# Kernel tuning notes

Hardware: AMD Instinct MI355X
Metric: run time of the kernel (lower is better)

Reference implementation:

```python
import jax, jax.numpy as jnp
import numpy as np

HEADS = 8
EPS = 1e-5


def _layernorm(x, g, b):
    mu = jnp.mean(x, axis=-1, keepdims=True)
    var = jnp.mean(jnp.square(x - mu), axis=-1, keepdims=True)
    return (x - mu) * jax.lax.rsqrt(var + EPS) * g + b


def setup_inputs() -> dict:
    key = jax.random.key(0)
    ks = jax.random.split(key, 10)
    B, S, D = 4, 2048, 256
    d_ff = 2 * D
    s = 0.02
    return {
        "x": jax.random.normal(ks[0], (B, S, D), dtype=jnp.float32),
        "ln1_g": jnp.ones((D,), jnp.float32),
        "ln1_b": jnp.zeros((D,), jnp.float32),
        "w_qkv": jax.random.normal(ks[1], (3 * D, D), jnp.float32) * s,
        "b_qkv": jnp.zeros((3 * D,), jnp.float32),
        "w_proj": jax.random.normal(ks[2], (D, D), jnp.float32) * s,
        "b_proj": jnp.zeros((D,), jnp.float32),
        "ln2_g": jnp.ones((D,), jnp.float32),
        "ln2_b": jnp.zeros((D,), jnp.float32),
        "w1": jax.random.normal(ks[3], (d_ff, D), jnp.float32) * s,
        "b1": jnp.zeros((d_ff,), jnp.float32),
        "w2": jax.random.normal(ks[4], (D, d_ff), jnp.float32) * s,
        "b2": jnp.zeros((D,), jnp.float32),
    }


def reference(x, ln1_g, ln1_b, w_qkv, b_qkv, w_proj, b_proj,
              ln2_g, ln2_b, w1, b1, w2, b2):
    B, S, D = x.shape
    H = HEADS
    dh = D // H
    scale = dh ** -0.5

    # --- attention sublayer (pre-LN) ---
    y = _layernorm(x, ln1_g, ln1_b)
    qkv = y @ w_qkv.T + b_qkv                       # [B,S,3D]
    qkv = qkv.reshape(B, S, 3, H, dh)
    q = jnp.transpose(qkv[:, :, 0], (0, 2, 1, 3))   # [B,H,S,dh]
    k = jnp.transpose(qkv[:, :, 1], (0, 2, 1, 3))
    v = jnp.transpose(qkv[:, :, 2], (0, 2, 1, 3))
    attn = jax.nn.softmax(jnp.einsum('bhsd,bhtd->bhst', q, k) * scale, axis=-1)
    ctx = jnp.einsum('bhst,bhtd->bhsd', attn, v)    # [B,H,S,dh]
    ctx = jnp.transpose(ctx, (0, 2, 1, 3)).reshape(B, S, D)
    x = x + ctx @ w_proj.T + b_proj

    # --- FFN sublayer (pre-LN) ---
    y = _layernorm(x, ln2_g, ln2_b)
    h = jax.nn.silu(y @ w1.T + b1)                  # [B,S,2D]
    x = x + h @ w2.T + b2
    return x
```

## Files before the change

### kernel.cpp

```cpp
#include <hip/hip_runtime.h>
#include <cstddef>

constexpr int kB   = 4;
constexpr int kS   = 2048;
constexpr int kD   = 256;
constexpr int kH   = 8;
constexpr int kDH  = 32;
constexpr int kDFF = 512;
constexpr int kM   = kB * kS;
constexpr float kEps = 1e-5f;
constexpr float kScaleL2E = 0.17677669529663687f * 1.4426950408889634f;

typedef float f32x4  __attribute__((ext_vector_type(4)));
typedef short bf16x8 __attribute__((ext_vector_type(8)));
typedef unsigned short u16;
typedef unsigned int   u32;

__device__ inline u16 f2bf(float x) {
    union { float f; unsigned u; } c; c.f = x;
    const unsigned r = c.u + 0x7fffu + ((c.u >> 16) & 1u);
    return (u16)(r >> 16);
}

__device__ inline u32 pk_trunc(float lo, float hi) {
    union { float f; u32 u; } a, b; a.f = lo; b.f = hi;
    return __builtin_amdgcn_perm(b.u, a.u, 0x07060302u);
}

__device__ inline size_t pkoff(int row, int col, int nkb) {
    return ((size_t)(row >> 4) * nkb + (col >> 5)) * 512
         + (row & 15) * 32 + (col & 31);
}

__global__ __launch_bounds__(256)
void conv_w_kernel(const float* __restrict__ wq, const float* __restrict__ wp,
                   const float* __restrict__ w1, const float* __restrict__ w2,
                   u16* __restrict__ dst)
{
    const int e0 = (blockIdx.x * 256 + threadIdx.x) * 4;
    const float* src; int off, K, base;
    if (e0 < 196608)      { src = wq; off = e0;          K = 256; base = 0; }
    else if (e0 < 262144) { src = wp; off = e0 - 196608; K = 256; base = 196608; }
    else if (e0 < 393216) { src = w1; off = e0 - 262144; K = 256; base = 262144; }
    else                  { src = w2; off = e0 - 393216; K = 512; base = 393216; }
    const float4 v = *(const float4*)&src[off];
    const int n = off / K, k = off - n * K;
    const size_t po = pkoff(n, k, K >> 5);
    *(ushort4*)&dst[base + po] = make_ushort4(f2bf(v.x), f2bf(v.y), f2bf(v.z), f2bf(v.w));
}

__global__ __launch_bounds__(256)
void ln_kernel(const float* __restrict__ x, const float* __restrict__ g,
               const float* __restrict__ b, u16* __restrict__ y)
{
    const int wave = threadIdx.x >> 6;
    const int lane = threadIdx.x & 63;
    const int row  = blockIdx.x * 4 + wave;
    const float4 v = *(const float4*)&x[(size_t)row * kD + lane * 4];
    float s1 = (v.x + v.y) + (v.z + v.w);
    float s2 = (v.x * v.x + v.y * v.y) + (v.z * v.z + v.w * v.w);
    #pragma unroll
    for (int off = 1; off < 64; off <<= 1) {
        s1 += __shfl_xor(s1, off);
        s2 += __shfl_xor(s2, off);
    }
    const float mu  = s1 * (1.0f / kD);
    const float var = s2 * (1.0f / kD) - mu * mu;
    const float inv = rsqrtf(var + kEps);
    const float4 g4 = *(const float4*)&g[lane * 4];
    const float4 b4 = *(const float4*)&b[lane * 4];
    *(ushort4*)&y[pkoff(row, lane * 4, kD >> 5)] = make_ushort4(
        f2bf((v.x - mu) * inv * g4.x + b4.x),
        f2bf((v.y - mu) * inv * g4.y + b4.y),
        f2bf((v.z - mu) * inv * g4.z + b4.z),
        f2bf((v.w - mu) * inv * g4.w + b4.w));
}

template<int NI, int OUTMODE, bool RES, int KTOT>
__global__ __launch_bounds__(256)
void gemm_pk(const u16* __restrict__ Ap, const u16* __restrict__ Wp,
             const float* __restrict__ bias, const float* __restrict__ res,
             float* __restrict__ Cf, u16* __restrict__ Cb,
             u16* __restrict__ KbP, u16* __restrict__ VtP, int N)
{
    constexpr int NK = KTOT / 32;
    const int tid  = threadIdx.x;
    const int wave = tid >> 6;
    const int lane = tid & 63;
    const int quad = lane >> 4;
    const int l16  = lane & 15;
    const int m0 = blockIdx.x * 128;
    const int n0 = blockIdx.y * (NI * 16);
    const int fo = l16 * 32 + quad * 8;

    f32x4 acc[2][NI];
    #pragma unroll
    for (int mt = 0; mt < 2; ++mt)
        #pragma unroll
        for (int ni = 0; ni < NI; ++ni) acc[mt][ni] = {0.f, 0.f, 0.f, 0.f};

    const u16* a0p = Ap + (size_t)((m0 >> 4) + wave)     * NK * 512 + fo;
    const u16* a1p = Ap + (size_t)((m0 >> 4) + 4 + wave) * NK * 512 + fo;
    const u16* wp  = Wp + (size_t)(n0 >> 4)              * NK * 512 + fo;

    #pragma unroll 2
    for (int k = 0; k < NK; ++k) {
        const bf16x8 a0 = *(const bf16x8*)&a0p[k * 512];
        const bf16x8 a1 = *(const bf16x8*)&a1p[k * 512];
        #pragma unroll
        for (int ni = 0; ni < NI; ++ni) {
            const bf16x8 wf = *(const bf16x8*)&wp[((size_t)ni * NK + k) * 512];
            acc[0][ni] = __builtin_amdgcn_mfma_f32_16x16x32_bf16(a0, wf, acc[0][ni], 0, 0, 0);
            acc[1][ni] = __builtin_amdgcn_mfma_f32_16x16x32_bf16(a1, wf, acc[1][ni], 0, 0, 0);
        }
    }

    #pragma unroll
    for (int mt = 0; mt < 2; ++mt) {
        #pragma unroll
        for (int ni = 0; ni < NI; ++ni) {
            const float bias_v = bias[n0 + ni * 16 + l16];
            #pragma unroll
            for (int r = 0; r < 4; ++r) {
                const int m = m0 + mt * 64 + wave * 16 + quad * 4 + r;
                const int n = n0 + ni * 16 + l16;
                float v = acc[mt][ni][r] + bias_v;
                if (OUTMODE == 0) {
                    if (RES) v += res[(size_t)m * N + n];
                    Cf[(size_t)m * N + n] = v;
                } else if (OUTMODE == 1) {
                    v = v / (1.0f + __expf(-v));
                    Cb[pkoff(m, n, kDFF >> 5)] = f2bf(v);
                } else {
                    const int rgn = n0 >> 8;
                    const int nl  = n & 255;
                    const int hh  = nl >> 5, dh = nl & 31;
                    const int bb  = m >> 11, s = m & (kS - 1);
                    const int bh  = bb * kH + hh;
                    if (rgn == 0)
                        Cb[((size_t)bh * kS + s) * kDH + dh] = f2bf(v * kScaleL2E);
                    else if (rgn == 1)
                        KbP[((size_t)bh * kS + s) * kDH + dh] = f2bf(v);
                    else {
                        const int so = s & 31;
                        const int vq = (so >> 2) & 3;
                        const int vj = (so & 3) | (((so >> 4) & 1) << 2);
                        VtP[(((size_t)bh * (kS / 32) + (s >> 5)) * 4 + vq) * 256
                            + dh * 8 + vj] = f2bf(v);
                    }
                }
            }
        }
    }
}

__global__ __launch_bounds__(256)
void attn_kernel(const u16* __restrict__ Qb, const u16* __restrict__ Kb,
                 const u16* __restrict__ Vp, u16* __restrict__ ctx)
{
    __shared__ float cbuf[2][64 * 33];
    const int tid  = threadIdx.x;
    const int wave = tid >> 6;
    const int lane = tid & 63;
    const int quad = lane >> 4;
    const int l16  = lane & 15;
    const int h = blockIdx.y;
    const int b = blockIdx.z;
    const int bh = b * kH + h;
    const int qsub = wave >> 1;
    const int half = wave & 1;
    const int q0 = blockIdx.x * 128 + qsub * 64;

    bf16x8 aq[4];
    #pragma unroll
    for (int qb = 0; qb < 4; ++qb)
        aq[qb] = *(const bf16x8*)
            &Qb[((size_t)bh * kS + q0 + qb * 16 + l16) * kDH + quad * 8];

    const u16* Kbase = Kb + (size_t)bh * kS * kDH;
    const u16* Vbase = Vp + (size_t)bh * (kS * 32);

    f32x4 O[4][2] = {};
    f32x4 lsum[4] = {};
    const f32x4 zz = {0.f, 0.f, 0.f, 0.f};
    union { u32 u[4]; bf16x8 v; } ones;
    ones.u[0] = ones.u[1] = ones.u[2] = ones.u[3] = 0x3F803F80u;

    auto load_tile = [&](int kt, bf16x8 (&kf)[4], bf16x8 (&vf)[2][2]) {
        #pragma unroll
        for (int kg = 0; kg < 4; ++kg)
            kf[kg] = *(const bf16x8*)
                &Kbase[(size_t)(kt + kg * 16 + l16) * kDH + quad * 8];
        #pragma unroll
        for (int ks = 0; ks < 2; ++ks)
            #pragma unroll
            for (int nf = 0; nf < 2; ++nf)
                vf[ks][nf] = *(const bf16x8*)
                    &Vbase[(size_t)(((kt >> 5) + ks) * 4 + quad) * 1024
                           + (nf * 16 + l16) * 8];
    };

    auto comp_tile = [&](bf16x8 (&kf)[4], bf16x8 (&vf)[2][2]) {
        #pragma unroll
        for (int qb = 0; qb < 4; ++qb) {
            f32x4 S0 = __builtin_amdgcn_mfma_f32_16x16x32_bf16(kf[0], aq[qb], zz, 0, 0, 0);
            f32x4 S1 = __builtin_amdgcn_mfma_f32_16x16x32_bf16(kf[1], aq[qb], zz, 0, 0, 0);
            f32x4 S2 = __builtin_amdgcn_mfma_f32_16x16x32_bf16(kf[2], aq[qb], zz, 0, 0, 0);
            f32x4 S3 = __builtin_amdgcn_mfma_f32_16x16x32_bf16(kf[3], aq[qb], zz, 0, 0, 0);

            union { u32 u[4]; bf16x8 v; } pA0, pA1;
            pA0.u[0] = pk_trunc(__builtin_amdgcn_exp2f(S0[0]), __builtin_amdgcn_exp2f(S0[1]));
            pA0.u[1] = pk_trunc(__builtin_amdgcn_exp2f(S0[2]), __builtin_amdgcn_exp2f(S0[3]));
            pA0.u[2] = pk_trunc(__builtin_amdgcn_exp2f(S1[0]), __builtin_amdgcn_exp2f(S1[1]));
            pA0.u[3] = pk_trunc(__builtin_amdgcn_exp2f(S1[2]), __builtin_amdgcn_exp2f(S1[3]));
            pA1.u[0] = pk_trunc(__builtin_amdgcn_exp2f(S2[0]), __builtin_amdgcn_exp2f(S2[1]));
            pA1.u[1] = pk_trunc(__builtin_amdgcn_exp2f(S2[2]), __builtin_amdgcn_exp2f(S2[3]));
            pA1.u[2] = pk_trunc(__builtin_amdgcn_exp2f(S3[0]), __builtin_amdgcn_exp2f(S3[1]));
            pA1.u[3] = pk_trunc(__builtin_amdgcn_exp2f(S3[2]), __builtin_amdgcn_exp2f(S3[3]));

            lsum[qb] = __builtin_amdgcn_mfma_f32_16x16x32_bf16(pA0.v, ones.v, lsum[qb], 0, 0, 0);
            lsum[qb] = __builtin_amdgcn_mfma_f32_16x16x32_bf16(pA1.v, ones.v, lsum[qb], 0, 0, 0);

            O[qb][0] = __builtin_amdgcn_mfma_f32_16x16x32_bf16(pA0.v, vf[0][0], O[qb][0], 0, 0, 0);
            O[qb][1] = __builtin_amdgcn_mfma_f32_16x16x32_bf16(pA0.v, vf[0][1], O[qb][1], 0, 0, 0);
            O[qb][0] = __builtin_amdgcn_mfma_f32_16x16x32_bf16(pA1.v, vf[1][0], O[qb][0], 0, 0, 0);
            O[qb][1] = __builtin_amdgcn_mfma_f32_16x16x32_bf16(pA1.v, vf[1][1], O[qb][1], 0, 0, 0);
        }
    };

    const int kbeg = half * (kS / 2);
    #pragma unroll 1
    for (int t2 = 0; t2 < 8; ++t2) {
        const int ktA = kbeg + t2 * 128;
        bf16x8 kfA[4], vfA[2][2], kfB[4], vfB[2][2];
        load_tile(ktA,      kfA, vfA);
        load_tile(ktA + 64, kfB, vfB);
        comp_tile(kfA, vfA);
        comp_tile(kfB, vfB);
    }

    float* cb = cbuf[qsub];
    if (half == 1) {
        #pragma unroll
        for (int qb = 0; qb < 4; ++qb)
            #pragma unroll
            for (int r = 0; r < 4; ++r) {
                const int row = qb * 16 + quad * 4 + r;
                cb[row * 33 + l16]      = O[qb][0][r];
                cb[row * 33 + 16 + l16] = O[qb][1][r];
                if (l16 == 0)
                    cb[row * 33 + 32] = lsum[qb][r];
            }
    }
    __syncthreads();
    if (half == 0) {
        #pragma unroll
        for (int qb = 0; qb < 4; ++qb)
            #pragma unroll
            for (int r = 0; r < 4; ++r) {
                const int row = qb * 16 + quad * 4 + r;
                const float lq  = lsum[qb][r] + cb[row * 33 + 32];
                const float inv = 1.0f / lq;
                const float o0 = O[qb][0][r] + cb[row * 33 + l16];
                const float o1 = O[qb][1][r] + cb[row * 33 + 16 + l16];
                const int q = q0 + row;
                const int mrow = b * kS + q;
                u16* crow = ctx + ((size_t)(mrow >> 4) * (kD >> 5) + h) * 512
                          + (mrow & 15) * 32;
                crow[l16]      = f2bf(o0 * inv);
                crow[16 + l16] = f2bf(o1 * inv);
            }
    }
}

extern "C" void kernel_launch(void* const* d_in, const int* in_sizes, int n_in,
                              void* d_out, int out_size, void* d_ws, size_t ws_size,
                              hipStream_t stream)
{
    const float* x      = (const float*)d_in[0];
    const float* ln1_g  = (const float*)d_in[1];
    const float* ln1_b  = (const float*)d_in[2];
    const float* w_qkv  = (const float*)d_in[3];
    const float* b_qkv  = (const float*)d_in[4];
    const float* w_proj = (const float*)d_in[5];
    const float* b_proj = (const float*)d_in[6];
    const float* ln2_g  = (const float*)d_in[7];
    const float* ln2_b  = (const float*)d_in[8];
    const float* w1     = (const float*)d_in[9];
    const float* b1     = (const float*)d_in[10];
    const float* w2     = (const float*)d_in[11];
    const float* b2     = (const float*)d_in[12];
    float* out = (float*)d_out;

    char* ws = (char*)d_ws;
    u16* Qb  = (u16*)ws;
    u16* Kb  = (u16*)(ws + ((size_t)4  << 20));
    u16* Vp  = (u16*)(ws + ((size_t)8  << 20));
    u16* ctx = (u16*)(ws + ((size_t)12 << 20));
    u16* y   = (u16*)(ws + ((size_t)16 << 20));
    u16* h   = (u16*)ws;
    u16* Wb  = (u16*)(ws + ((size_t)20 << 20));
    u16* wqb = Wb;
    u16* wpb = Wb + 196608;
    u16* w1b = Wb + 262144;
    u16* w2b = Wb + 393216;

    const dim3 blk(256);

    conv_w_kernel<<<dim3(512), blk, 0, stream>>>(w_qkv, w_proj, w1, w2, Wb);
    ln_kernel<<<dim3(kM / 4), blk, 0, stream>>>(x, ln1_g, ln1_b, y);
    gemm_pk<4, 2, false, 256><<<dim3(kM / 128, 12), blk, 0, stream>>>(
        y, wqb, b_qkv, nullptr, nullptr, Qb, Kb, Vp, 0);
    attn_kernel<<<dim3(kS / 128, kH, kB), blk, 0, stream>>>(Qb, Kb, Vp, ctx);
    gemm_pk<2, 0, true, 256><<<dim3(kM / 128, kD / 32), blk, 0, stream>>>(
        ctx, wpb, b_proj, x, out, nullptr, nullptr, nullptr, kD);
    ln_kernel<<<dim3(kM / 4), blk, 0, stream>>>(out, ln2_g, ln2_b, y);
    gemm_pk<4, 1, false, 256><<<dim3(kM / 128, kDFF / 64), blk, 0, stream>>>(
        y, w1b, b1, nullptr, nullptr, h, nullptr, nullptr, kDFF);
    gemm_pk<2, 0, true, 512><<<dim3(kM / 128, kD / 32), blk, 0, stream>>>(
        h, w2b, b2, out, out, nullptr, nullptr, nullptr, kD);
}
```

Before: 162.1 us.

## Keep weight fragments in registers across M tiles and fuse weight conversion into LN

The GEMM kernel now preloads each block's full weight fragments (NI x NK bf16x8) into registers once, then loops over two M tiles, reusing them instead of re-reading weights from global memory for every k step. The N tile width is reduced (NI 4->2 or 2->1) to keep register use manageable, and the grid changes accordingly. The weight conversion is folded into the first LayerNorm launch as extra blocks, saving one kernel launch. The register-held weights raise VGPR pressure and may cut occupancy, and A-tile loads are still streamed from global memory.

```diff
diff --git a/kernel.cpp b/kernel.cpp
--- a/kernel.cpp
+++ b/kernel.cpp
@@ -8,6 +8,7 @@
 constexpr int kDH  = 32;
 constexpr int kDFF = 512;
 constexpr int kM   = kB * kS;
+constexpr int kMT  = kM / 128;
 constexpr float kEps = 1e-5f;
 constexpr float kScaleL2E = 0.17677669529663687f * 1.4426950408889634f;
 
@@ -33,26 +34,26 @@
 }
 
 __global__ __launch_bounds__(256)
-void conv_w_kernel(const float* __restrict__ wq, const float* __restrict__ wp,
-                   const float* __restrict__ w1, const float* __restrict__ w2,
-                   u16* __restrict__ dst)
+void prep_kernel(const float* __restrict__ x, const float* __restrict__ g,
+                 const float* __restrict__ b, u16* __restrict__ y,
+                 const float* __restrict__ wq, const float* __restrict__ wp,
+                 const float* __restrict__ w1, const float* __restrict__ w2,
+                 u16* __restrict__ wdst)
 {
-    const int e0 = (blockIdx.x * 256 + threadIdx.x) * 4;
-    const float* src; int off, K, base;
-    if (e0 < 196608)      { src = wq; off = e0;          K = 256; base = 0; }
-    else if (e0 < 262144) { src = wp; off = e0 - 196608; K = 256; base = 196608; }
-    else if (e0 < 393216) { src = w1; off = e0 - 262144; K = 256; base = 262144; }
-    else                  { src = w2; off = e0 - 393216; K = 512; base = 393216; }
-    const float4 v = *(const float4*)&src[off];
-    const int n = off / K, k = off - n * K;
-    const size_t po = pkoff(n, k, K >> 5);
-    *(ushort4*)&dst[base + po] = make_ushort4(f2bf(v.x), f2bf(v.y), f2bf(v.z), f2bf(v.w));
-}
-
-__global__ __launch_bounds__(256)
-void ln_kernel(const float* __restrict__ x, const float* __restrict__ g,
-               const float* __restrict__ b, u16* __restrict__ y)
-{
+    if (blockIdx.x >= kM / 4) {
+        const int e0 = ((blockIdx.x - kM / 4) * 256 + threadIdx.x) * 4;
+        const float* src; int off, K, base;
+        if (e0 < 196608)      { src = wq; off = e0;          K = 256; base = 0; }
+        else if (e0 < 262144) { src = wp; off = e0 - 196608; K = 256; base = 196608; }
+        else if (e0 < 393216) { src = w1; off = e0 - 262144; K = 256; base = 262144; }
+        else                  { src = w2; off = e0 - 393216; K = 512; base = 393216; }
+        const float4 v = *(const float4*)&src[off];
+        const int n = off / K, k = off - n * K;
+        const size_t po = pkoff(n, k, K >> 5);
+        *(ushort4*)&wdst[base + po] =
+            make_ushort4(f2bf(v.x), f2bf(v.y), f2bf(v.z), f2bf(v.w));
+        return;
+    }
     const int wave = threadIdx.x >> 6;
     const int lane = threadIdx.x & 63;
     const int row  = blockIdx.x * 4 + wave;
@@ -76,77 +77,91 @@
         f2bf((v.w - mu) * inv * g4.w + b4.w));
 }
 
-template<int NI, int OUTMODE, bool RES, int KTOT>
+template<int NI, int OUTMODE, bool RES, int KTOT, int MT>
 __global__ __launch_bounds__(256)
-void gemm_pk(const u16* __restrict__ Ap, const u16* __restrict__ Wp,
+void gemm_ps(const u16* __restrict__ Ap, const u16* __restrict__ Wp,
              const float* __restrict__ bias, const float* __restrict__ res,
              float* __restrict__ Cf, u16* __restrict__ Cb,
              u16* __restrict__ KbP, u16* __restrict__ VtP, int N)
 {
     constexpr int NK = KTOT / 32;
+    constexpr int GX = kMT / MT;
     const int tid  = threadIdx.x;
     const int wave = tid >> 6;
     const int lane = tid & 63;
     const int quad = lane >> 4;
     const int l16  = lane & 15;
-    const int m0 = blockIdx.x * 128;
     const int n0 = blockIdx.y * (NI * 16);
     const int fo = l16 * 32 + quad * 8;
 
-    f32x4 acc[2][NI];
+    bf16x8 wfr[NI][NK];
     #pragma unroll
-    for (int mt = 0; mt < 2; ++mt)
-        #pragma unroll
-        for (int ni = 0; ni < NI; ++ni) acc[mt][ni] = {0.f, 0.f, 0.f, 0.f};
-
-    const u16* a0p = Ap + (size_t)((m0 >> 4) + wave)     * NK * 512 + fo;
-    const u16* a1p = Ap + (size_t)((m0 >> 4) + 4 + wave) * NK * 512 + fo;
-    const u16* wp  = Wp + (size_t)(n0 >> 4)              * NK * 512 + fo;
-
-    #pragma unroll 2
-    for (int k = 0; k < NK; ++k) {
-        const bf16x8 a0 = *(const bf16x8*)&a0p[k * 512];
-        const bf16x8 a1 = *(const bf16x8*)&a1p[k * 512];
-        #pragma unroll
-        for (int ni = 0; ni < NI; ++ni) {
-            const bf16x8 wf = *(const bf16x8*)&wp[((size_t)ni * NK + k) * 512];
-            acc[0][ni] = __builtin_amdgcn_mfma_f32_16x16x32_bf16(a0, wf, acc[0][ni], 0, 0, 0);
-            acc[1][ni] = __builtin_amdgcn_mfma_f32_16x16x32_bf16(a1, wf, acc[1][ni], 0, 0, 0);
+    for (int ni = 0; ni < NI; ++ni)
+        #pragma unroll
+        for (int k = 0; k < NK; ++k)
+            wfr[ni][k] = *(const bf16x8*)
+                &Wp[(size_t)((n0 >> 4) + ni) * NK * 512 + (size_t)k * 512 + fo];
+
+    float biasv[NI];
+    #pragma unroll
+    for (int ni = 0; ni < NI; ++ni) biasv[ni] = bias[n0 + ni * 16 + l16];
+
+    #pragma unroll 1
+    for (int t = 0; t < MT; ++t) {
+        const int m0 = (blockIdx.x + t * GX) * 128;
+
+        f32x4 acc[2][NI];
+        #pragma unroll
+        for (int mt = 0; mt < 2; ++mt)
+            #pragma unroll
+            for (int ni = 0; ni < NI; ++ni) acc[mt][ni] = {0.f, 0.f, 0.f, 0.f};
+
+        const u16* a0p = Ap + (size_t)((m0 >> 4) + wave)     * NK * 512 + fo;
+        const u16* a1p = Ap + (size_t)((m0 >> 4) + 4 + wave) * NK * 512 + fo;
+
+        #pragma unroll 4
+        for (int k = 0; k < NK; ++k) {
+            const bf16x8 a0 = *(const bf16x8*)&a0p[(size_t)k * 512];
+            const bf16x8 a1 = *(const bf16x8*)&a1p[(size_t)k * 512];
+            #pragma unroll
+            for (int ni = 0; ni < NI; ++ni) {
+                acc[0][ni] = __builtin_amdgcn_mfma_f32_16x16x32_bf16(a0, wfr[ni][k], acc[0][ni], 0, 0, 0);
+                acc[1][ni] = __builtin_amdgcn_mfma_f32_16x16x32_bf16(a1, wfr[ni][k], acc[1][ni], 0, 0, 0);
+            }
         }
-    }
-
-    #pragma unroll
-    for (int mt = 0; mt < 2; ++mt) {
-        #pragma unroll
-        for (int ni = 0; ni < NI; ++ni) {
-            const float bias_v = bias[n0 + ni * 16 + l16];
-            #pragma unroll
-            for (int r = 0; r < 4; ++r) {
-                const int m = m0 + mt * 64 + wave * 16 + quad * 4 + r;
-                const int n = n0 + ni * 16 + l16;
-                float v = acc[mt][ni][r] + bias_v;
-                if (OUTMODE == 0) {
-                    if (RES) v += res[(size_t)m * N + n];
-                    Cf[(size_t)m * N + n] = v;
-                } else if (OUTMODE == 1) {
-                    v = v / (1.0f + __expf(-v));
-                    Cb[pkoff(m, n, kDFF >> 5)] = f2bf(v);
-                } else {
-                    const int rgn = n0 >> 8;
-                    const int nl  = n & 255;
-                    const int hh  = nl >> 5, dh = nl & 31;
-                    const int bb  = m >> 11, s = m & (kS - 1);
-                    const int bh  = bb * kH + hh;
-                    if (rgn == 0)
-                        Cb[((size_t)bh * kS + s) * kDH + dh] = f2bf(v * kScaleL2E);
-                    else if (rgn == 1)
-                        KbP[((size_t)bh * kS + s) * kDH + dh] = f2bf(v);
-                    else {
-                        const int so = s & 31;
-                        const int vq = (so >> 2) & 3;
-                        const int vj = (so & 3) | (((so >> 4) & 1) << 2);
-                        VtP[(((size_t)bh * (kS / 32) + (s >> 5)) * 4 + vq) * 256
-                            + dh * 8 + vj] = f2bf(v);
+
+        #pragma unroll
+        for (int mt = 0; mt < 2; ++mt) {
+            #pragma unroll
+            for (int ni = 0; ni < NI; ++ni) {
+                #pragma unroll
+                for (int r = 0; r < 4; ++r) {
+                    const int m = m0 + mt * 64 + wave * 16 + quad * 4 + r;
+                    const int n = n0 + ni * 16 + l16;
+                    float v = acc[mt][ni][r] + biasv[ni];
+                    if (OUTMODE == 0) {
+                        if (RES) v += res[(size_t)m * N + n];
+                        Cf[(size_t)m * N + n] = v;
+                    } else if (OUTMODE == 1) {
+                        v = v / (1.0f + __expf(-v));
+                        Cb[pkoff(m, n, kDFF >> 5)] = f2bf(v);
+                    } else {
+                        const int rgn = n0 >> 8;
+                        const int nl  = n & 255;
+                        const int hh  = nl >> 5, dh = nl & 31;
+                        const int bb  = m >> 11, s = m & (kS - 1);
+                        const int bh  = bb * kH + hh;
+                        if (rgn == 0)
+                            Cb[((size_t)bh * kS + s) * kDH + dh] = f2bf(v * kScaleL2E);
+                        else if (rgn == 1)
+                            KbP[((size_t)bh * kS + s) * kDH + dh] = f2bf(v);
+                        else {
+                            const int so = s & 31;
+                            const int vq = (so >> 2) & 3;
+                            const int vj = (so & 3) | (((so >> 4) & 1) << 2);
+                            VtP[(((size_t)bh * (kS / 32) + (s >> 5)) * 4 + vq) * 256
+                                + dh * 8 + vj] = f2bf(v);
+                        }
                     }
                 }
             }
@@ -307,16 +322,17 @@
 
     const dim3 blk(256);
 
-    conv_w_kernel<<<dim3(512), blk, 0, stream>>>(w_qkv, w_proj, w1, w2, Wb);
-    ln_kernel<<<dim3(kM / 4), blk, 0, stream>>>(x, ln1_g, ln1_b, y);
-    gemm_pk<4, 2, false, 256><<<dim3(kM / 128, 12), blk, 0, stream>>>(
+    prep_kernel<<<dim3(kM / 4 + 512), blk, 0, stream>>>(
+        x, ln1_g, ln1_b, y, w_qkv, w_proj, w1, w2, Wb);
+    gemm_ps<2, 2, false, 256, 2><<<dim3(kMT / 2, 24), blk, 0, stream>>>(
         y, wqb, b_qkv, nullptr, nullptr, Qb, Kb, Vp, 0);
     attn_kernel<<<dim3(kS / 128, kH, kB), blk, 0, stream>>>(Qb, Kb, Vp, ctx);
-    gemm_pk<2, 0, true, 256><<<dim3(kM / 128, kD / 32), blk, 0, stream>>>(
+    gemm_ps<2, 0, true, 256, 2><<<dim3(kMT / 2, 8), blk, 0, stream>>>(
         ctx, wpb, b_proj, x, out, nullptr, nullptr, nullptr, kD);
-    ln_kernel<<<dim3(kM / 4), blk, 0, stream>>>(out, ln2_g, ln2_b, y);
-    gemm_pk<4, 1, false, 256><<<dim3(kM / 128, kDFF / 64), blk, 0, stream>>>(
+    prep_kernel<<<dim3(kM / 4), blk, 0, stream>>>(
+        out, ln2_g, ln2_b, y, nullptr, nullptr, nullptr, nullptr, nullptr);
+    gemm_ps<2, 1, false, 256, 2><<<dim3(kMT / 2, 16), blk, 0, stream>>>(
         y, w1b, b1, nullptr, nullptr, h, nullptr, nullptr, kDFF);
-    gemm_pk<2, 0, true, 512><<<dim3(kM / 128, kD / 32), blk, 0, stream>>>(
+    gemm_ps<1, 0, true, 512, 2><<<dim3(kMT / 2, 16), blk, 0, stream>>>(
         h, w2b, b2, out, out, nullptr, nullptr, nullptr, kD);
 }
```

Result: slower. 207.1 us (+27.8%).

## Fuse weight conversion with LN1, and output projection with residual and LN2

Applied to the files above, without the earlier changes.

Merges the weight bf16 conversion and the first layernorm into one launch by giving extra blocks the conversion work. Replaces the projection GEMM plus separate LN2 kernel with a single kernel in which each wave computes 16 full rows of 256 columns via MFMA, adds bias and residual, writes out, then does row reduction and LN2 in registers. This removes two launches and the round trip of the projection output through memory before LN2. In exchange, the new projection kernel reads weights straight from global memory without LDS tiling and uses a 128-block grid, which may cut occupancy and weight reuse.

```diff
diff --git a/kernel.cpp b/kernel.cpp
--- a/kernel.cpp
+++ b/kernel.cpp
@@ -33,26 +33,26 @@
 }
 
 __global__ __launch_bounds__(256)
-void conv_w_kernel(const float* __restrict__ wq, const float* __restrict__ wp,
-                   const float* __restrict__ w1, const float* __restrict__ w2,
-                   u16* __restrict__ dst)
-{
-    const int e0 = (blockIdx.x * 256 + threadIdx.x) * 4;
-    const float* src; int off, K, base;
-    if (e0 < 196608)      { src = wq; off = e0;          K = 256; base = 0; }
-    else if (e0 < 262144) { src = wp; off = e0 - 196608; K = 256; base = 196608; }
-    else if (e0 < 393216) { src = w1; off = e0 - 262144; K = 256; base = 262144; }
-    else                  { src = w2; off = e0 - 393216; K = 512; base = 393216; }
-    const float4 v = *(const float4*)&src[off];
-    const int n = off / K, k = off - n * K;
-    const size_t po = pkoff(n, k, K >> 5);
-    *(ushort4*)&dst[base + po] = make_ushort4(f2bf(v.x), f2bf(v.y), f2bf(v.z), f2bf(v.w));
-}
-
-__global__ __launch_bounds__(256)
-void ln_kernel(const float* __restrict__ x, const float* __restrict__ g,
-               const float* __restrict__ b, u16* __restrict__ y)
-{
+void prep_kernel(const float* __restrict__ x, const float* __restrict__ g,
+                 const float* __restrict__ b, u16* __restrict__ y,
+                 const float* __restrict__ wq, const float* __restrict__ wp,
+                 const float* __restrict__ w1, const float* __restrict__ w2,
+                 u16* __restrict__ wdst)
+{
+    if (blockIdx.x >= kM / 4) {
+        const int e0 = ((blockIdx.x - kM / 4) * 256 + threadIdx.x) * 4;
+        const float* src; int off, K, base;
+        if (e0 < 196608)      { src = wq; off = e0;          K = 256; base = 0; }
+        else if (e0 < 262144) { src = wp; off = e0 - 196608; K = 256; base = 196608; }
+        else if (e0 < 393216) { src = w1; off = e0 - 262144; K = 256; base = 262144; }
+        else                  { src = w2; off = e0 - 393216; K = 512; base = 393216; }
+        const float4 v = *(const float4*)&src[off];
+        const int n = off / K, k = off - n * K;
+        const size_t po = pkoff(n, k, K >> 5);
+        *(ushort4*)&wdst[base + po] =
+            make_ushort4(f2bf(v.x), f2bf(v.y), f2bf(v.z), f2bf(v.w));
+        return;
+    }
     const int wave = threadIdx.x >> 6;
     const int lane = threadIdx.x & 63;
     const int row  = blockIdx.x * 4 + wave;
@@ -155,6 +155,70 @@
 }
 
 __global__ __launch_bounds__(256)
+void proj_ln2_kernel(const u16* __restrict__ ctx, const u16* __restrict__ Wp,
+                     const float* __restrict__ bias, const float* __restrict__ x,
+                     const float* __restrict__ g, const float* __restrict__ bb,
+                     float* __restrict__ out, u16* __restrict__ y)
+{
+    const int tid  = threadIdx.x;
+    const int wave = tid >> 6;
+    const int lane = tid & 63;
+    const int quad = lane >> 4;
+    const int l16  = lane & 15;
+    const int tr   = blockIdx.x * 4 + wave;
+    const int fo   = l16 * 32 + quad * 8;
+
+    f32x4 acc[16];
+    #pragma unroll
+    for (int ni = 0; ni < 16; ++ni) acc[ni] = {0.f, 0.f, 0.f, 0.f};
+
+    const u16* ap = ctx + (size_t)tr * 8 * 512 + fo;
+    #pragma unroll 2
+    for (int k = 0; k < 8; ++k) {
+        const bf16x8 a = *(const bf16x8*)&ap[k * 512];
+        #pragma unroll
+        for (int ni = 0; ni < 16; ++ni) {
+            const bf16x8 wf = *(const bf16x8*)&Wp[((size_t)ni * 8 + k) * 512 + fo];
+            acc[ni] = __builtin_amdgcn_mfma_f32_16x16x32_bf16(a, wf, acc[ni], 0, 0, 0);
+        }
+    }
+
+    float bv[16], gv[16], bbv[16];
+    #pragma unroll
+    for (int ni = 0; ni < 16; ++ni) {
+        bv[ni]  = bias[ni * 16 + l16];
+        gv[ni]  = g[ni * 16 + l16];
+        bbv[ni] = bb[ni * 16 + l16];
+    }
+
+    const int m0 = tr * 16;
+    #pragma unroll
+    for (int r = 0; r < 4; ++r) {
+        const int m = m0 + quad * 4 + r;
+        float v[16], s1 = 0.f, s2 = 0.f;
+        #pragma unroll
+        for (int ni = 0; ni < 16; ++ni) {
+            v[ni] = acc[ni][r] + bv[ni] + x[(size_t)m * kD + ni * 16 + l16];
+            out[(size_t)m * kD + ni * 16 + l16] = v[ni];
+            s1 += v[ni];
+            s2 += v[ni] * v[ni];
+        }
+        s1 += __shfl_xor(s1, 1); s2 += __shfl_xor(s2, 1);
+        s1 += __shfl_xor(s1, 2); s2 += __shfl_xor(s2, 2);
+        s1 += __shfl_xor(s1, 4); s2 += __shfl_xor(s2, 4);
+        s1 += __shfl_xor(s1, 8); s2 += __shfl_xor(s2, 8);
+        const float mu  = s1 * (1.0f / kD);
+        const float var = s2 * (1.0f / kD) - mu * mu;
+        const float inv = rsqrtf(var + kEps);
+        u16* yb = y + (size_t)tr * 8 * 512 + (quad * 4 + r) * 32 + l16;
+        #pragma unroll
+        for (int ni = 0; ni < 16; ++ni)
+            yb[(ni >> 1) * 512 + (ni & 1) * 16] =
+                f2bf((v[ni] - mu) * inv * gv[ni] + bbv[ni]);
+    }
+}
+
+__global__ __launch_bounds__(256)
 void attn_kernel(const u16* __restrict__ Qb, const u16* __restrict__ Kb,
                  const u16* __restrict__ Vp, u16* __restrict__ ctx)
 {
@@ -307,14 +371,13 @@
 
     const dim3 blk(256);
 
-    conv_w_kernel<<<dim3(512), blk, 0, stream>>>(w_qkv, w_proj, w1, w2, Wb);
-    ln_kernel<<<dim3(kM / 4), blk, 0, stream>>>(x, ln1_g, ln1_b, y);
+    prep_kernel<<<dim3(kM / 4 + 512), blk, 0, stream>>>(
+        x, ln1_g, ln1_b, y, w_qkv, w_proj, w1, w2, Wb);
     gemm_pk<4, 2, false, 256><<<dim3(kM / 128, 12), blk, 0, stream>>>(
         y, wqb, b_qkv, nullptr, nullptr, Qb, Kb, Vp, 0);
     attn_kernel<<<dim3(kS / 128, kH, kB), blk, 0, stream>>>(Qb, Kb, Vp, ctx);
-    gemm_pk<2, 0, true, 256><<<dim3(kM / 128, kD / 32), blk, 0, stream>>>(
-        ctx, wpb, b_proj, x, out, nullptr, nullptr, nullptr, kD);
-    ln_kernel<<<dim3(kM / 4), blk, 0, stream>>>(out, ln2_g, ln2_b, y);
+    proj_ln2_kernel<<<dim3(kM / 64), blk, 0, stream>>>(
+        ctx, wpb, b_proj, x, ln2_g, ln2_b, out, y);
     gemm_pk<4, 1, false, 256><<<dim3(kM / 128, kDFF / 64), blk, 0, stream>>>(
         y, w1b, b1, nullptr, nullptr, h, nullptr, nullptr, kDFF);
     gemm_pk<2, 0, true, 512><<<dim3(kM / 128, kD / 32), blk, 0, stream>>>(
```

Result: no change. 162.4 us (+0.2%).
